# Kernel optimization log

Measured on AMD Instinct MI355X. Metric: run time of the kernel, lower is better.

Reference implementation:

```python
import jax, jax.numpy as jnp
import numpy as np

C = 128
GROUPS = 8
EPS = 1e-5


def setup_inputs() -> dict:
    key = jax.random.key(0)
    ks = jax.random.split(key, 7)
    x = jax.random.normal(ks[0], (8, C, 256, 256), dtype=jnp.float32)
    gn_w = jax.random.normal(ks[1], (C,), dtype=jnp.float32) * 0.02 + 1.0
    gn_b = jax.random.normal(ks[2], (C,), dtype=jnp.float32) * 0.02
    w1 = jax.random.normal(ks[3], (C, C), dtype=jnp.float32) * (1.0 / np.sqrt(C))
    b1 = jax.random.normal(ks[4], (C,), dtype=jnp.float32) * 0.02
    w2 = jax.random.normal(ks[5], (C, C), dtype=jnp.float32) * (1.0 / np.sqrt(C))
    b2 = jax.random.normal(ks[6], (C,), dtype=jnp.float32) * 0.02
    return {"x": x, "gn_w": gn_w, "gn_b": gn_b, "w1": w1, "b1": b1, "w2": w2, "b2": b2}


def reference(x, gn_w, gn_b, w1, b1, w2, b2):
    # fft2 -> ifft2(..).real round-trip (faithful to original; numerically ~identity)
    x_ifft = jnp.fft.ifft2(jnp.fft.fft2(x, axes=(-2, -1)), axes=(-2, -1)).real.astype(x.dtype)

    # GroupNorm over (C//G, H, W) per group
    B, Ch, H, W = x_ifft.shape
    g = x_ifft.reshape(B, GROUPS, Ch // GROUPS, H, W)
    mean = g.mean(axis=(2, 3, 4), keepdims=True)
    var = g.var(axis=(2, 3, 4), keepdims=True)
    xn = ((g - mean) * jax.lax.rsqrt(var + EPS)).reshape(B, Ch, H, W)
    xn = xn * gn_w[None, :, None, None] + gn_b[None, :, None, None]

    # 1x1 conv -> ReLU -> 1x1 conv (as channel GEMMs)
    h = jnp.einsum('oc,bchw->bohw', w1, xn) + b1[None, :, None, None]
    h = jax.nn.relu(h)
    ffn = jnp.einsum('oc,bchw->bohw', w2, h) + b2[None, :, None, None]
    return x_ifft + ffn
```

## Files before the change

### kernel.cpp

```cpp
#include <hip/hip_runtime.h>

typedef __attribute__((ext_vector_type(8))) short s16x8;
typedef __attribute__((ext_vector_type(4))) float f32x4;

#define CCH 128

__device__ __forceinline__ ushort f2bf(float f) {
  uint u = __float_as_uint(f);
  u += 0x7fffu + ((u >> 16) & 1u);
  return (ushort)(u >> 16);
}
__device__ __forceinline__ float bf2f(ushort u) {
  return __uint_as_float(((uint)u) << 16);
}

__device__ __forceinline__ int swz(int row, int col) {
  return (row << 7) | (col ^ ((row & 7) << 3));
}

__global__ __launch_bounds__(256) void pass1_stats_tr(const float* __restrict__ x,
                                                      ushort* __restrict__ xb,
                                                      float2* __restrict__ partials) {
  __shared__ ushort sT[256 * CCH];
  __shared__ float ws1[4][8], ws2[4][8];
  const int t = threadIdx.x;
  const int b = blockIdx.x >> 8;
  const int p0 = (blockIdx.x & 255) << 8;
  const int wv = t >> 6, lane = t & 63;
  const int px4 = lane << 2;
  float sg1[8], sg2[8];
#pragma unroll
  for (int g = 0; g < 8; ++g) { sg1[g] = 0.f; sg2[g] = 0.f; }

  const float* xbase = x + (((size_t)b * CCH) << 16) + p0;
#pragma unroll
  for (int i = 0; i < 8; ++i) {
    const int ch = i * 16 + wv * 4;
    float4 v[4];
#pragma unroll
    for (int j = 0; j < 4; ++j)
      v[j] = *(const float4*)(xbase + (((size_t)(ch + j)) << 16) + px4);
#pragma unroll
    for (int j = 0; j < 4; ++j) {
      sg1[i] += v[j].x + v[j].y + v[j].z + v[j].w;
      sg2[i] += v[j].x * v[j].x + v[j].y * v[j].y + v[j].z * v[j].z + v[j].w * v[j].w;
    }
#pragma unroll
    for (int k = 0; k < 4; ++k) {
      const int row = px4 + k;
      const int gs = (i * 4 + wv) ^ (((row >> 3) & 15) << 1);
      ushort4 pk;
      pk.x = f2bf(((const float*)&v[0])[k]);
      pk.y = f2bf(((const float*)&v[1])[k]);
      pk.z = f2bf(((const float*)&v[2])[k]);
      pk.w = f2bf(((const float*)&v[3])[k]);
      *(ushort4*)&sT[row * CCH + gs * 4] = pk;
    }
  }
#pragma unroll
  for (int g = 0; g < 8; ++g) {
    float a = sg1[g], q = sg2[g];
#pragma unroll
    for (int off = 32; off > 0; off >>= 1) {
      a += __shfl_down(a, off);
      q += __shfl_down(q, off);
    }
    if (lane == 0) { ws1[wv][g] = a; ws2[wv][g] = q; }
  }
  __syncthreads();
  if (t < 8) {
    float a = ws1[0][t] + ws1[1][t] + ws1[2][t] + ws1[3][t];
    float q = ws2[0][t] + ws2[1][t] + ws2[2][t] + ws2[3][t];
    partials[blockIdx.x * 8 + t] = (float2){a, q};
  }
  const int c16 = t & 15, pr = t >> 4;
  ushort* dst = xb + ((size_t)((b << 16) + p0)) * CCH;
#pragma unroll
  for (int s = 0; s < 16; ++s) {
    const int row = s * 16 + pr;
    const int gs = (c16 * 2) ^ (((row >> 3) & 15) << 1);
    *(s16x8*)&dst[(size_t)row * CCH + c16 * 8] = *(const s16x8*)&sT[row * CCH + gs * 4];
  }
}

__global__ void stats_finalize2(const float2* __restrict__ partials,
                                const float* __restrict__ gn_w,
                                const float* __restrict__ gn_b,
                                float* __restrict__ scale, float* __restrict__ shift) {
  const int t = threadIdx.x;
  const int b = t >> 3, g = t & 7;
  float s1 = 0.f, s2 = 0.f;
  for (int c = 0; c < 256; ++c) {
    float2 p = partials[(b * 256 + c) * 8 + g];
    s1 += p.x;
    s2 += p.y;
  }
  const float invN = 1.0f / 1048576.0f;
  const float mean = s1 * invN;
  const float var = s2 * invN - mean * mean;
  const float rstd = rsqrtf(var + 1e-5f);
  for (int i = 0; i < 16; ++i) {
    const int c = g * 16 + i;
    const float sc = rstd * gn_w[c];
    scale[b * CCH + c] = sc;
    shift[b * CCH + c] = gn_b[c] - mean * sc;
  }
}

__global__ __launch_bounds__(256) void prep_w2(const float* __restrict__ w2,
                                               ushort* __restrict__ w2b) {
  int i = blockIdx.x * 256 + threadIdx.x;
  float4 a = ((const float4*)w2)[i];
  ushort4 o;
  o.x = f2bf(a.x); o.y = f2bf(a.y); o.z = f2bf(a.z); o.w = f2bf(a.w);
  ((ushort4*)w2b)[i] = o;
}

__global__ __launch_bounds__(128) void fold_w1(const float* __restrict__ w1,
                                               const float* __restrict__ b1,
                                               const float* __restrict__ scale,
                                               const float* __restrict__ shift,
                                               ushort* __restrict__ W1b,
                                               float* __restrict__ c1) {
  const int b = blockIdx.x >> 7, o = blockIdx.x & 127, c = threadIdx.x;
  const float wv = w1[o * CCH + c];
  W1b[(b << 14) + o * CCH + c] = f2bf(wv * scale[b * CCH + c]);
  float s = wv * shift[b * CCH + c];
#pragma unroll
  for (int off = 32; off > 0; off >>= 1) s += __shfl_down(s, off);
  __shared__ float tmp[2];
  if ((threadIdx.x & 63) == 0) tmp[threadIdx.x >> 6] = s;
  __syncthreads();
  if (threadIdx.x == 0) c1[(b << 7) + o] = tmp[0] + tmp[1] + b1[o];
}

__global__ __launch_bounds__(256, 4) void mlp_tiled(
    const ushort* __restrict__ xb, const ushort* __restrict__ W1b,
    const ushort* __restrict__ w2b, const float* __restrict__ c1,
    const float* __restrict__ b2, float* __restrict__ out) {
  __shared__ ushort sB[128 * CCH];
  const int t = threadIdx.x;
  const int b = blockIdx.x >> 9;
  const int p0 = (blockIdx.x & 511) << 7;
  const int lane = t & 63;
  const int wv = t >> 6;
  const int fl = lane & 15;
  const int fh = lane >> 4;

  const ushort* src = xb + ((size_t)((b << 16) + p0)) * CCH;
#pragma unroll
  for (int i = 0; i < 8; ++i) {
    const int u = i * 256 + t;
    const int px = u >> 4;
    const int ch = (u & 15) * 8;
    const s16x8 v = *(const s16x8*)(src + px * CCH + ch);
    *(s16x8*)&sB[swz(px, ch)] = v;
  }
  __syncthreads();

  f32x4 acc[2][8];
#pragma unroll
  for (int f = 0; f < 2; ++f)
#pragma unroll
    for (int j = 0; j < 8; ++j) acc[f][j] = (f32x4){0.f, 0.f, 0.f, 0.f};

  const ushort* w1p = W1b + (b << 14);
#pragma unroll
  for (int k0 = 0; k0 < 128; k0 += 32) {
    const int kb = k0 + fh * 8;
    const s16x8 a0 = *(const s16x8*)(w1p + (wv * 32 + fl) * CCH + kb);
    const s16x8 a1 = *(const s16x8*)(w1p + (wv * 32 + 16 + fl) * CCH + kb);
#pragma unroll
    for (int j = 0; j < 8; ++j) {
      const s16x8 bf = *(const s16x8*)&sB[swz(j * 16 + fl, kb)];
      acc[0][j] = __builtin_amdgcn_mfma_f32_16x16x32_bf16(a0, bf, acc[0][j], 0, 0, 0);
      acc[1][j] = __builtin_amdgcn_mfma_f32_16x16x32_bf16(a1, bf, acc[1][j], 0, 0, 0);
    }
  }
  __syncthreads();

  const float* c1b = c1 + (b << 7);
#pragma unroll
  for (int f = 0; f < 2; ++f) {
    const int ob = wv * 32 + f * 16 + fh * 4;
    const float4 cc = *(const float4*)(c1b + ob);
#pragma unroll
    for (int j = 0; j < 8; ++j) {
      ushort4 pk;
      pk.x = f2bf(fmaxf(acc[f][j][0] + cc.x, 0.f));
      pk.y = f2bf(fmaxf(acc[f][j][1] + cc.y, 0.f));
      pk.z = f2bf(fmaxf(acc[f][j][2] + cc.z, 0.f));
      pk.w = f2bf(fmaxf(acc[f][j][3] + cc.w, 0.f));
      *(ushort4*)&sB[swz(j * 16 + fl, ob)] = pk;
    }
  }
  __syncthreads();

  f32x4 acc2[2][8];
#pragma unroll
  for (int f = 0; f < 2; ++f)
#pragma unroll
    for (int j = 0; j < 8; ++j) acc2[f][j] = (f32x4){0.f, 0.f, 0.f, 0.f};

#pragma unroll
  for (int k0 = 0; k0 < 128; k0 += 32) {
    const int kb = k0 + fh * 8;
    const s16x8 a0 = *(const s16x8*)(w2b + (wv * 32 + fl) * CCH + kb);
    const s16x8 a1 = *(const s16x8*)(w2b + (wv * 32 + 16 + fl) * CCH + kb);
#pragma unroll
    for (int j = 0; j < 8; ++j) {
      const s16x8 bf = *(const s16x8*)&sB[swz(j * 16 + fl, kb)];
      acc2[0][j] = __builtin_amdgcn_mfma_f32_16x16x32_bf16(a0, bf, acc2[0][j], 0, 0, 0);
      acc2[1][j] = __builtin_amdgcn_mfma_f32_16x16x32_bf16(a1, bf, acc2[1][j], 0, 0, 0);
    }
  }

#pragma unroll
  for (int f = 0; f < 2; ++f) {
    const int ob = wv * 32 + f * 16 + fh * 4;
    const float4 bb = *(const float4*)(b2 + ob);
#pragma unroll
    for (int j = 0; j < 8; ++j) {
      const int pcol = j * 16 + fl;
      const ushort4 rx = *(const ushort4*)(src + pcol * CCH + ob);
      const size_t base = (((size_t)(b * CCH + ob)) << 16) + p0 + pcol;
      out[base] = bf2f(rx.x) + acc2[f][j][0] + bb.x;
      out[base + ((size_t)1 << 16)] = bf2f(rx.y) + acc2[f][j][1] + bb.y;
      out[base + ((size_t)2 << 16)] = bf2f(rx.z) + acc2[f][j][2] + bb.z;
      out[base + ((size_t)3 << 16)] = bf2f(rx.w) + acc2[f][j][3] + bb.w;
    }
  }
}

extern "C" void kernel_launch(void* const* d_in, const int* in_sizes, int n_in,
                              void* d_out, int out_size, void* d_ws, size_t ws_size,
                              hipStream_t stream) {
  const float* x    = (const float*)d_in[0];
  const float* gn_w = (const float*)d_in[1];
  const float* gn_b = (const float*)d_in[2];
  const float* w1   = (const float*)d_in[3];
  const float* b1   = (const float*)d_in[4];
  const float* w2   = (const float*)d_in[5];
  const float* b2   = (const float*)d_in[6];
  float* out = (float*)d_out;
  char* ws = (char*)d_ws;

  const size_t XB_BYTES = (size_t)8 * 65536 * CCH * 2;
  ushort* xbuf  = (ushort*)ws;
  float2* parts = (float2*)(ws + XB_BYTES);
  float* scale  = (float*)(ws + XB_BYTES + 131072);
  float* shift  = (float*)(ws + XB_BYTES + 135168);
  ushort* w2b   = (ushort*)(ws + XB_BYTES + 139264);
  ushort* W1b   = (ushort*)(ws + XB_BYTES + 172032);
  float* c1     = (float*)(ws + XB_BYTES + 434176);

  hipLaunchKernelGGL(pass1_stats_tr, dim3(2048), dim3(256), 0, stream, x, xbuf, parts);
  hipLaunchKernelGGL(prep_w2, dim3(16), dim3(256), 0, stream, w2, w2b);
  hipLaunchKernelGGL(stats_finalize2, dim3(1), dim3(64), 0, stream, parts, gn_w, gn_b, scale, shift);
  hipLaunchKernelGGL(fold_w1, dim3(1024), dim3(128), 0, stream, w1, b1, scale, shift, W1b, c1);
  hipLaunchKernelGGL(mlp_tiled, dim3(4096), dim3(256), 0, stream, xbuf, W1b, w2b, c1, b2, out);
}
```

Before: 234.0 us.

## Restructure MLP kernel so each wave owns a 32-pixel slice, staging output through LDS

The MLP kernel now gives each wave its own 32-pixel slice of activations in LDS and computes all 128 output channels for it. This removes the block-wide barriers between the two GEMMs, and the residual is read from LDS before being overwritten by the hidden activations. The output is transposed through LDS so global stores become coalesced 16-byte writes along the pixel dimension. Block indices are also remapped to interleave batches across the grid. In exchange, weight A-fragments are now loaded from global or L2 per wave for all 8 output tiles, which raises weight traffic.

```diff
diff --git a/kernel.cpp b/kernel.cpp
--- a/kernel.cpp
+++ b/kernel.cpp
@@ -12,10 +12,6 @@
 }
 __device__ __forceinline__ float bf2f(ushort u) {
   return __uint_as_float(((uint)u) << 16);
-}
-
-__device__ __forceinline__ int swz(int row, int col) {
-  return (row << 7) | (col ^ ((row & 7) << 3));
 }
 
 __global__ __launch_bounds__(256) void pass1_stats_tr(const float* __restrict__ x,
@@ -134,100 +130,125 @@
   if (threadIdx.x == 0) c1[(b << 7) + o] = tmp[0] + tmp[1] + b1[o];
 }
 
-__global__ __launch_bounds__(256, 4) void mlp_tiled(
+__global__ __launch_bounds__(256, 4) void wavepipe(
     const ushort* __restrict__ xb, const ushort* __restrict__ W1b,
     const ushort* __restrict__ w2b, const float* __restrict__ c1,
     const float* __restrict__ b2, float* __restrict__ out) {
-  __shared__ ushort sB[128 * CCH];
-  const int t = threadIdx.x;
-  const int b = blockIdx.x >> 9;
-  const int p0 = (blockIdx.x & 511) << 7;
-  const int lane = t & 63;
-  const int wv = t >> 6;
-  const int fl = lane & 15;
-  const int fh = lane >> 4;
-
-  const ushort* src = xb + ((size_t)((b << 16) + p0)) * CCH;
+  __shared__ ushort sl[4][4096];
+  float* sF = (float*)&sl[0][0];
+  const int t = threadIdx.x, lane = t & 63, wv = t >> 6;
+  const int fl = lane & 15, fh = lane >> 4;
+  const int blk = ((blockIdx.x & 7) << 9) | (blockIdx.x >> 3);
+  const int b = blk >> 9;
+  const int p0 = (blk & 511) << 7;
+  const int pw = p0 + wv * 32;
+  ushort* slice = &sl[wv][0];
+
+  const ushort* src = xb + ((size_t)((b << 16) + pw)) * CCH;
 #pragma unroll
   for (int i = 0; i < 8; ++i) {
-    const int u = i * 256 + t;
-    const int px = u >> 4;
-    const int ch = (u & 15) * 8;
-    const s16x8 v = *(const s16x8*)(src + px * CCH + ch);
-    *(s16x8*)&sB[swz(px, ch)] = v;
-  }
-  __syncthreads();
-
-  f32x4 acc[2][8];
-#pragma unroll
-  for (int f = 0; f < 2; ++f)
-#pragma unroll
-    for (int j = 0; j < 8; ++j) acc[f][j] = (f32x4){0.f, 0.f, 0.f, 0.f};
+    const int px = i * 4 + (lane >> 4);
+    const int g = lane & 15;
+    const s16x8 v = *(const s16x8*)(src + px * CCH + g * 8);
+    *(s16x8*)&slice[px * CCH + ((g ^ (px & 7)) * 8)] = v;
+  }
+
+  f32x4 acc[8][2];
+#pragma unroll
+  for (int to = 0; to < 8; ++to)
+#pragma unroll
+    for (int tp = 0; tp < 2; ++tp) acc[to][tp] = (f32x4){0.f, 0.f, 0.f, 0.f};
 
   const ushort* w1p = W1b + (b << 14);
 #pragma unroll
-  for (int k0 = 0; k0 < 128; k0 += 32) {
-    const int kb = k0 + fh * 8;
-    const s16x8 a0 = *(const s16x8*)(w1p + (wv * 32 + fl) * CCH + kb);
-    const s16x8 a1 = *(const s16x8*)(w1p + (wv * 32 + 16 + fl) * CCH + kb);
-#pragma unroll
-    for (int j = 0; j < 8; ++j) {
-      const s16x8 bf = *(const s16x8*)&sB[swz(j * 16 + fl, kb)];
-      acc[0][j] = __builtin_amdgcn_mfma_f32_16x16x32_bf16(a0, bf, acc[0][j], 0, 0, 0);
-      acc[1][j] = __builtin_amdgcn_mfma_f32_16x16x32_bf16(a1, bf, acc[1][j], 0, 0, 0);
-    }
-  }
-  __syncthreads();
-
+  for (int k0 = 0; k0 < 4; ++k0) {
+    const int kb = k0 * 32 + fh * 8;
+    const int gb = k0 * 4 + fh;
+    const s16x8 bt0 = *(const s16x8*)&slice[fl * CCH + ((gb ^ (fl & 7)) * 8)];
+    const s16x8 bt1 = *(const s16x8*)&slice[(16 + fl) * CCH + ((gb ^ (fl & 7)) * 8)];
+#pragma unroll
+    for (int to = 0; to < 8; ++to) {
+      const s16x8 a = *(const s16x8*)(w1p + (to * 16 + fl) * CCH + kb);
+      acc[to][0] = __builtin_amdgcn_mfma_f32_16x16x32_bf16(a, bt0, acc[to][0], 0, 0, 0);
+      acc[to][1] = __builtin_amdgcn_mfma_f32_16x16x32_bf16(a, bt1, acc[to][1], 0, 0, 0);
+    }
+  }
+
+  ushort4 rx[8][2];
   const float* c1b = c1 + (b << 7);
 #pragma unroll
+  for (int to = 0; to < 8; ++to) {
+    const int ob = to * 16 + fh * 4;
+    const float4 cc = *(const float4*)(c1b + ob);
+    const int gq = to * 2 + (fh >> 1);
+    const int hq = (fh & 1) * 4;
+#pragma unroll
+    for (int tp = 0; tp < 2; ++tp) {
+      const int px = tp * 16 + fl;
+      ushort* p = &slice[px * CCH + (gq ^ (px & 7)) * 8 + hq];
+      rx[to][tp] = *(const ushort4*)p;
+      ushort4 pk;
+      pk.x = f2bf(fmaxf(acc[to][tp][0] + cc.x, 0.f));
+      pk.y = f2bf(fmaxf(acc[to][tp][1] + cc.y, 0.f));
+      pk.z = f2bf(fmaxf(acc[to][tp][2] + cc.z, 0.f));
+      pk.w = f2bf(fmaxf(acc[to][tp][3] + cc.w, 0.f));
+      *(ushort4*)p = pk;
+    }
+  }
+
+  f32x4 acc2[8][2];
+#pragma unroll
+  for (int to = 0; to < 8; ++to)
+#pragma unroll
+    for (int tp = 0; tp < 2; ++tp) acc2[to][tp] = (f32x4){0.f, 0.f, 0.f, 0.f};
+
+#pragma unroll
+  for (int k0 = 0; k0 < 4; ++k0) {
+    const int kb = k0 * 32 + fh * 8;
+    const int gb = k0 * 4 + fh;
+    const s16x8 bt0 = *(const s16x8*)&slice[fl * CCH + ((gb ^ (fl & 7)) * 8)];
+    const s16x8 bt1 = *(const s16x8*)&slice[(16 + fl) * CCH + ((gb ^ (fl & 7)) * 8)];
+#pragma unroll
+    for (int to = 0; to < 8; ++to) {
+      const s16x8 a = *(const s16x8*)(w2b + (to * 16 + fl) * CCH + kb);
+      acc2[to][0] = __builtin_amdgcn_mfma_f32_16x16x32_bf16(a, bt0, acc2[to][0], 0, 0, 0);
+      acc2[to][1] = __builtin_amdgcn_mfma_f32_16x16x32_bf16(a, bt1, acc2[to][1], 0, 0, 0);
+    }
+  }
+
+  const int pxb = wv * 32;
+#pragma unroll
   for (int f = 0; f < 2; ++f) {
-    const int ob = wv * 32 + f * 16 + fh * 4;
-    const float4 cc = *(const float4*)(c1b + ob);
-#pragma unroll
-    for (int j = 0; j < 8; ++j) {
-      ushort4 pk;
-      pk.x = f2bf(fmaxf(acc[f][j][0] + cc.x, 0.f));
-      pk.y = f2bf(fmaxf(acc[f][j][1] + cc.y, 0.f));
-      pk.z = f2bf(fmaxf(acc[f][j][2] + cc.z, 0.f));
-      pk.w = f2bf(fmaxf(acc[f][j][3] + cc.w, 0.f));
-      *(ushort4*)&sB[swz(j * 16 + fl, ob)] = pk;
-    }
-  }
-  __syncthreads();
-
-  f32x4 acc2[2][8];
-#pragma unroll
-  for (int f = 0; f < 2; ++f)
-#pragma unroll
-    for (int j = 0; j < 8; ++j) acc2[f][j] = (f32x4){0.f, 0.f, 0.f, 0.f};
-
-#pragma unroll
-  for (int k0 = 0; k0 < 128; k0 += 32) {
-    const int kb = k0 + fh * 8;
-    const s16x8 a0 = *(const s16x8*)(w2b + (wv * 32 + fl) * CCH + kb);
-    const s16x8 a1 = *(const s16x8*)(w2b + (wv * 32 + 16 + fl) * CCH + kb);
-#pragma unroll
-    for (int j = 0; j < 8; ++j) {
-      const s16x8 bf = *(const s16x8*)&sB[swz(j * 16 + fl, kb)];
-      acc2[0][j] = __builtin_amdgcn_mfma_f32_16x16x32_bf16(a0, bf, acc2[0][j], 0, 0, 0);
-      acc2[1][j] = __builtin_amdgcn_mfma_f32_16x16x32_bf16(a1, bf, acc2[1][j], 0, 0, 0);
-    }
-  }
-
-#pragma unroll
-  for (int f = 0; f < 2; ++f) {
-    const int ob = wv * 32 + f * 16 + fh * 4;
-    const float4 bb = *(const float4*)(b2 + ob);
-#pragma unroll
-    for (int j = 0; j < 8; ++j) {
-      const int pcol = j * 16 + fl;
-      const ushort4 rx = *(const ushort4*)(src + pcol * CCH + ob);
-      const size_t base = (((size_t)(b * CCH + ob)) << 16) + p0 + pcol;
-      out[base] = bf2f(rx.x) + acc2[f][j][0] + bb.x;
-      out[base + ((size_t)1 << 16)] = bf2f(rx.y) + acc2[f][j][1] + bb.y;
-      out[base + ((size_t)2 << 16)] = bf2f(rx.z) + acc2[f][j][2] + bb.z;
-      out[base + ((size_t)3 << 16)] = bf2f(rx.w) + acc2[f][j][3] + bb.w;
+    asm volatile("s_waitcnt lgkmcnt(0)" ::: "memory");
+    __builtin_amdgcn_s_barrier();
+#pragma unroll
+    for (int to4 = 0; to4 < 4; ++to4) {
+      const int to = f * 4 + to4;
+      const int chb = to * 16 + fh * 4;
+      const float4 bb = *(const float4*)(b2 + chb);
+#pragma unroll
+      for (int tp = 0; tp < 2; ++tp) {
+        const int px = pxb + tp * 16 + fl;
+        const int g = px >> 2, e = px & 3;
+        float v0 = acc2[to][tp][0] + bb.x + bf2f(rx[to][tp].x);
+        float v1 = acc2[to][tp][1] + bb.y + bf2f(rx[to][tp].y);
+        float v2 = acc2[to][tp][2] + bb.z + bf2f(rx[to][tp].z);
+        float v3 = acc2[to][tp][3] + bb.w + bf2f(rx[to][tp].w);
+        const int r0 = to4 * 16 + fh * 4;
+        sF[(r0 + 0) * 128 + ((g ^ ((r0 + 0) & 7)) << 2) + e] = v0;
+        sF[(r0 + 1) * 128 + ((g ^ ((r0 + 1) & 7)) << 2) + e] = v1;
+        sF[(r0 + 2) * 128 + ((g ^ ((r0 + 2) & 7)) << 2) + e] = v2;
+        sF[(r0 + 3) * 128 + ((g ^ ((r0 + 3) & 7)) << 2) + e] = v3;
+      }
+    }
+    asm volatile("s_waitcnt lgkmcnt(0)" ::: "memory");
+    __builtin_amdgcn_s_barrier();
+#pragma unroll
+    for (int i = 0; i < 8; ++i) {
+      const int rd = wv * 16 + i * 2 + (lane >> 5);
+      const int g = lane & 31;
+      const f32x4 v = *(const f32x4*)&sF[rd * 128 + ((g ^ (rd & 7)) << 2)];
+      *(f32x4*)(out + (((size_t)(b * CCH + f * 64 + rd)) << 16) + p0 + g * 4) = v;
     }
   }
 }
@@ -245,18 +266,18 @@
   float* out = (float*)d_out;
   char* ws = (char*)d_ws;
 
-  const size_t XB_BYTES = (size_t)8 * 65536 * CCH * 2;
+  const size_t XB = (size_t)8 * 65536 * CCH * 2;
   ushort* xbuf  = (ushort*)ws;
-  float2* parts = (float2*)(ws + XB_BYTES);
-  float* scale  = (float*)(ws + XB_BYTES + 131072);
-  float* shift  = (float*)(ws + XB_BYTES + 135168);
-  ushort* w2b   = (ushort*)(ws + XB_BYTES + 139264);
-  ushort* W1b   = (ushort*)(ws + XB_BYTES + 172032);
-  float* c1     = (float*)(ws + XB_BYTES + 434176);
+  float2* parts = (float2*)(ws + XB);
+  float* scale  = (float*)(ws + XB + 131072);
+  float* shift  = (float*)(ws + XB + 135168);
+  ushort* w2b   = (ushort*)(ws + XB + 139264);
+  ushort* W1b   = (ushort*)(ws + XB + 172032);
+  float* c1     = (float*)(ws + XB + 434176);
 
   hipLaunchKernelGGL(pass1_stats_tr, dim3(2048), dim3(256), 0, stream, x, xbuf, parts);
-  hipLaunchKernelGGL(prep_w2, dim3(16), dim3(256), 0, stream, w2, w2b);
   hipLaunchKernelGGL(stats_finalize2, dim3(1), dim3(64), 0, stream, parts, gn_w, gn_b, scale, shift);
   hipLaunchKernelGGL(fold_w1, dim3(1024), dim3(128), 0, stream, w1, b1, scale, shift, W1b, c1);
-  hipLaunchKernelGGL(mlp_tiled, dim3(4096), dim3(256), 0, stream, xbuf, W1b, w2b, c1, b2, out);
-}
+  hipLaunchKernelGGL(prep_w2, dim3(16), dim3(256), 0, stream, w2, w2b);
+  hipLaunchKernelGGL(wavepipe, dim3(4096), dim3(256), 0, stream, xbuf, W1b, w2b, c1, b2, out);
+}
```

Result: slower. 323.6 us (+38.3%).
